# Performance work log

Measured on AMD Instinct MI355X. Metric: run time of the kernel, lower is better.

The kernel has to match this reference:

```python
import jax, jax.numpy as jnp
import numpy as np

ALPHA = 0.2  # LeakyReLU negative slope


def _pair_indices(N):
    # Faithful reproduction of the source's cat(dim=1)+view indexing quirk.
    # a_input[b, i, j, :F]  = h[b, idx(m0)] with m0 = 2*(i*N + j)
    # a_input[b, i, j, F:]  = h[b, idx(m1)] with m1 = m0 + 1
    # idx(m) = m // N            if m <  N*N   (first repeat: h_i blocks)
    #        = (m - N*N) % N     if m >= N*N   (second repeat: h_j tiling)
    i = jnp.arange(N, dtype=jnp.int32)[:, None]
    j = jnp.arange(N, dtype=jnp.int32)[None, :]
    m0 = 2 * (i * N + j)
    m1 = m0 + 1
    NN = N * N
    idx0 = jnp.where(m0 < NN, m0 // N, (m0 - NN) % N)
    idx1 = jnp.where(m1 < NN, m1 // N, (m1 - NN) % N)
    return idx0, idx1  # each [N, N] int32


def reference(inp, W, a):
    # inp: [B, N, Fin], W: [Fin, Fout], a: [2*Fout, 1]
    h = inp @ W                       # [B, N, F]
    B, N, F = h.shape
    a1 = a[:F, 0]                     # [F]
    a2 = a[F:, 0]                     # [F]
    # Decompose additive score: a_input @ a = a1.h_left + a2.h_right
    s1 = h @ a1                       # [B, N]
    s2 = h @ a2                       # [B, N]
    idx0, idx1 = _pair_indices(N)     # [N, N]
    score = s1[:, idx0] + s2[:, idx1]                     # [B, N, N]
    score = jax.nn.leaky_relu(score, negative_slope=ALPHA)
    attn = jax.nn.softmax(score, axis=1)                  # softmax over dim=1 as in source
    # dropout is identity in eval mode (dropout=0.0)
    h_prime = jnp.einsum('bij,bjf->bif', attn, h)         # [B, N, F]
    return jax.nn.elu(h_prime)                            # concat=True -> ELU


def setup_inputs() -> dict:
    B, N, Fin, Fout = 4, 4096, 128, 64
    key = jax.random.key(0)
    k1, k2, k3 = jax.random.split(key, 3)
    inp = jax.random.normal(k1, (B, N, Fin), dtype=jnp.float32)
    # xavier_uniform with gain=1.414
    gain = 1.414
    lim_W = gain * np.sqrt(6.0 / (Fin + Fout))
    W = jax.random.uniform(k2, (Fin, Fout), dtype=jnp.float32, minval=-lim_W, maxval=lim_W)
    lim_a = gain * np.sqrt(6.0 / (2 * Fout + 1))
    a = jax.random.uniform(k3, (2 * Fout, 1), dtype=jnp.float32, minval=-lim_a, maxval=lim_a)
    return {"inp": inp, "W": W, "a": a}
```

## Files before the change

kernel.cpp:

```cpp
#include <hip/hip_runtime.h>
#include <math.h>

#define ALPHA 0.2f

constexpr int BB   = 4;
constexpr int NN_  = 4096;
constexpr int HN   = 2048;
constexpr int FIN  = 128;
constexpr int FF   = 64;
constexpr int ROWS = BB * NN_;

constexpr size_t WS_H  = 0;
constexpr size_t WS_C  = (size_t)ROWS * FF;
constexpr size_t WS_E  = WS_C + ROWS;
constexpr size_t WS_A0 = WS_E + ROWS;
constexpr size_t WS_A1 = WS_A0 + (size_t)BB * FF;
constexpr size_t WS_U  = WS_A1 + (size_t)BB * FF;
constexpr size_t WS_M  = WS_U + (size_t)BB * FF;
constexpr size_t WS_WQ = WS_M + 2 * BB;

__global__ __launch_bounds__(256) void k1_gemm(const float* __restrict__ inp,
                                               const float* __restrict__ W,
                                               const float* __restrict__ a,
                                               float* __restrict__ ws) {
  const int tid  = threadIdx.x;
  const int lane = tid & 63;
  const int wv   = __builtin_amdgcn_readfirstlane(tid >> 6);
  __shared__ float rows_s[32 * FIN];

  float Wreg[FIN];
  #pragma unroll
  for (int k = 0; k < FIN; ++k) Wreg[k] = W[k * FF + lane];
  const float a1 = a[lane];
  const float a2 = a[FF + lane];
  const float asum = a1 + a2;

  const int rowbase = blockIdx.x * 32;
  const float4* src = reinterpret_cast<const float4*>(inp + (size_t)rowbase * FIN);
  float4* dst = reinterpret_cast<float4*>(rows_s);
  #pragma unroll
  for (int i = 0; i < 4; ++i) dst[tid + i * 256] = src[tid + i * 256];
  __syncthreads();

  float* hout = ws + WS_H;
  float* cout = ws + WS_C;
  float* eout = ws + WS_E;

  #pragma unroll
  for (int p = 0; p < 4; ++p) {
    const int lr0 = wv * 8 + 2 * p;
    const float* rp0 = rows_s + lr0 * FIN;
    const float* rp1 = rp0 + FIN;
    float h0 = 0.f, h0b = 0.f, h1 = 0.f, h1b = 0.f;
    #pragma unroll
    for (int k = 0; k < FIN; k += 4) {
      const float4 x0 = *reinterpret_cast<const float4*>(rp0 + k);
      const float4 x1 = *reinterpret_cast<const float4*>(rp1 + k);
      h0  = fmaf(x0.x, Wreg[k],     h0);
      h0b = fmaf(x0.y, Wreg[k + 1], h0b);
      h0  = fmaf(x0.z, Wreg[k + 2], h0);
      h0b = fmaf(x0.w, Wreg[k + 3], h0b);
      h1  = fmaf(x1.x, Wreg[k],     h1);
      h1b = fmaf(x1.y, Wreg[k + 1], h1b);
      h1  = fmaf(x1.z, Wreg[k + 2], h1);
      h1b = fmaf(x1.w, Wreg[k + 3], h1b);
    }
    const float H0 = h0 + h0b;
    const float H1 = h1 + h1b;
    const int r0 = rowbase + lr0;
    hout[(size_t)r0 * FF + lane] = H0;
    hout[(size_t)(r0 + 1) * FF + lane] = H1;

    float c0 = H0 * asum, e0 = H0 * a1;
    float c1 = H1 * asum, e1 = H1 * a2;
    #pragma unroll
    for (int s = 32; s >= 1; s >>= 1) {
      c0 += __shfl_xor(c0, s, 64);
      e0 += __shfl_xor(e0, s, 64);
      c1 += __shfl_xor(c1, s, 64);
      e1 += __shfl_xor(e1, s, 64);
    }
    if (lane == 0) {
      cout[r0] = c0;     eout[r0] = e0;
      cout[r0 + 1] = c1; eout[r0 + 1] = e1;
    }
  }
}

__global__ __launch_bounds__(1024) void k2_stats(float* __restrict__ ws) {
  const int b    = blockIdx.x;
  const int tid  = threadIdx.x;
  const int lane = tid & 63;
  const int w    = tid >> 6;
  const float* c = ws + WS_C + (size_t)b * NN_;
  const float* e = ws + WS_E + (size_t)b * NN_;
  __shared__ float redm[16][2];
  __shared__ float bc[4];

  const float4 cv = reinterpret_cast<const float4*>(c)[tid];
  const float l0 = cv.x > 0.f ? cv.x : ALPHA * cv.x;
  const float l1 = cv.y > 0.f ? cv.y : ALPHA * cv.y;
  const float l2 = cv.z > 0.f ? cv.z : ALPHA * cv.z;
  const float l3 = cv.w > 0.f ? cv.w : ALPHA * cv.w;
  float me = fmaxf(l0, l2), mo = fmaxf(l1, l3);
  #pragma unroll
  for (int s = 32; s >= 1; s >>= 1) {
    me = fmaxf(me, __shfl_xor(me, s, 64));
    mo = fmaxf(mo, __shfl_xor(mo, s, 64));
  }
  if (lane == 0) { redm[w][0] = me; redm[w][1] = mo; }
  __syncthreads();
  if (tid == 0) {
    float M0 = -INFINITY, M1 = -INFINITY;
    for (int i = 0; i < 16; ++i) {
      M0 = fmaxf(M0, redm[i][0]);
      M1 = fmaxf(M1, redm[i][1]);
    }
    bc[0] = M0; bc[1] = M1;
  }
  __syncthreads();
  const float M0 = bc[0], M1 = bc[1];
  float se = __expf(l0 - M0) + __expf(l2 - M0);
  float so = __expf(l1 - M1) + __expf(l3 - M1);
  #pragma unroll
  for (int s = 32; s >= 1; s >>= 1) {
    se += __shfl_xor(se, s, 64);
    so += __shfl_xor(so, s, 64);
  }
  __syncthreads();
  if (lane == 0) { redm[w][0] = se; redm[w][1] = so; }
  __syncthreads();
  if (tid == 0) {
    float P0 = 0.f, P1 = 0.f;
    for (int i = 0; i < 16; ++i) { P0 += redm[i][0]; P1 += redm[i][1]; }
    bc[2] = P0; bc[3] = P1;
    ws[WS_M + 2 * b]     = M0;
    ws[WS_M + 2 * b + 1] = M1;
  }
  __syncthreads();
  const float P0 = bc[2], P1 = bc[3];

  float4* wq = reinterpret_cast<float4*>(ws + WS_WQ) + (size_t)b * HN;
  #pragma unroll
  for (int i = 0; i < 2; ++i) {
    const int jp = tid + i * 1024;
    const float2 ev = reinterpret_cast<const float2*>(e)[jp];
    const float d = ev.x + ev.y;
    const float v = d > 0.f ? d : ALPHA * d;
    const float m0 = fmaxf(M0, v), m1 = fmaxf(M1, v);
    const float eM0 = __expf(M0 - m0), ev0 = __expf(v - m0);
    const float eM1 = __expf(M1 - m1), ev1 = __expf(v - m1);
    const float Z0 = eM0 * P0 + (float)HN * ev0;
    const float Z1 = eM1 * P1 + (float)HN * ev1;
    wq[jp] = make_float4(eM0 / Z0, ev0 / Z0, eM1 / Z1, ev1 / Z1);
  }
  if (tid < FF) {
    ws[WS_A0 + (size_t)b * FF + tid] = 0.f;
    ws[WS_A1 + (size_t)b * FF + tid] = 0.f;
    ws[WS_U  + (size_t)b * FF + tid] = 0.f;
  }
}

constexpr int NSEG = 32;
constexpr int SEGR = 128;

__global__ __launch_bounds__(256) void k3_colsum(float* __restrict__ ws) {
  const int b    = blockIdx.x >> 5;
  const int seg  = blockIdx.x & 31;
  const int tid  = threadIdx.x;
  const int lane = tid & 63;
  const int wv   = __builtin_amdgcn_readfirstlane(tid >> 6);
  const float* h = ws + WS_H + (size_t)b * NN_ * FF;
  const float4* wq = reinterpret_cast<const float4*>(ws + WS_WQ) + (size_t)b * HN;
  __shared__ float accbuf[4][2][64];

  const int j0 = seg * SEGR + wv * 32;
  float accA = 0.f, accU = 0.f;
  #pragma unroll 8
  for (int r = 0; r < 32; ++r) {
    const int j = j0 + r;
    const float hv = h[(size_t)j * FF + lane];
    const float4 q = wq[j & (HN - 1)];
    const float qa = (j < HN) ? q.x : q.z;
    const float qu = (j < HN) ? q.y : q.w;
    accA = fmaf(qa, hv, accA);
    accU = fmaf(qu, hv, accU);
  }
  accbuf[wv][0][lane] = accA;
  accbuf[wv][1][lane] = accU;
  __syncthreads();
  if (tid < 64) {
    const float sA = accbuf[0][0][tid] + accbuf[1][0][tid] + accbuf[2][0][tid] + accbuf[3][0][tid];
    const float sU = accbuf[0][1][tid] + accbuf[1][1][tid] + accbuf[2][1][tid] + accbuf[3][1][tid];
    float* A = ws + ((seg < NSEG / 2) ? WS_A0 : WS_A1) + (size_t)b * FF;
    atomicAdd(&A[tid], sA);
    atomicAdd(ws + WS_U + (size_t)b * FF + tid, sU);
  }
}

__global__ __launch_bounds__(256) void k4_out(const float* __restrict__ ws,
                                              float* __restrict__ out) {
  const int idx = blockIdx.x * 256 + threadIdx.x;
  const int b   = idx >> 16;
  const int rem = idx & 65535;
  const int i   = rem >> 4;
  const int fg  = rem & 15;
  float4 v;
  if (i < HN) {
    const float* c = ws + WS_C + (size_t)b * NN_;
    const float M0 = ws[WS_M + 2 * b];
    const float M1 = ws[WS_M + 2 * b + 1];
    float c0 = c[2 * i], c1 = c[2 * i + 1];
    c0 = c0 > 0.f ? c0 : ALPHA * c0;
    c1 = c1 > 0.f ? c1 : ALPHA * c1;
    const float al = __expf(c0 - M0);
    const float be = __expf(c1 - M1);
    const float4 A0v = reinterpret_cast<const float4*>(ws + WS_A0 + (size_t)b * FF)[fg];
    const float4 A1v = reinterpret_cast<const float4*>(ws + WS_A1 + (size_t)b * FF)[fg];
    v.x = al * A0v.x + be * A1v.x;
    v.y = al * A0v.y + be * A1v.y;
    v.z = al * A0v.z + be * A1v.z;
    v.w = al * A0v.w + be * A1v.w;
  } else {
    v = reinterpret_cast<const float4*>(ws + WS_U + (size_t)b * FF)[fg];
  }
  v.x = v.x > 0.f ? v.x : expm1f(v.x);
  v.y = v.y > 0.f ? v.y : expm1f(v.y);
  v.z = v.z > 0.f ? v.z : expm1f(v.z);
  v.w = v.w > 0.f ? v.w : expm1f(v.w);
  reinterpret_cast<float4*>(out)[idx] = v;
}

extern "C" void kernel_launch(void* const* d_in, const int* in_sizes, int n_in,
                              void* d_out, int out_size, void* d_ws, size_t ws_size,
                              hipStream_t stream) {
  (void)in_sizes; (void)n_in; (void)out_size; (void)ws_size;
  const float* inp = (const float*)d_in[0];
  const float* W   = (const float*)d_in[1];
  const float* a   = (const float*)d_in[2];
  float* out = (float*)d_out;
  float* ws  = (float*)d_ws;

  hipLaunchKernelGGL(k1_gemm,   dim3(ROWS / 32),        dim3(256),  0, stream, inp, W, a, ws);
  hipLaunchKernelGGL(k2_stats,  dim3(BB),               dim3(1024), 0, stream, ws);
  hipLaunchKernelGGL(k3_colsum, dim3(BB * NSEG),        dim3(256),  0, stream, ws);
  hipLaunchKernelGGL(k4_out,    dim3(ROWS * FF / 1024), dim3(256),  0, stream, ws, out);
}
```

Measured before the change: 34.99 us.

## Fuse four kernels into one persistent kernel with global atomic barriers

```diff
diff --git a/kernel.cpp b/kernel.cpp
--- a/kernel.cpp
+++ b/kernel.cpp
@@ -9,141 +9,152 @@
 constexpr int FIN  = 128;
 constexpr int FF   = 64;
 constexpr int ROWS = BB * NN_;
-
-constexpr size_t WS_H  = 0;
-constexpr size_t WS_C  = (size_t)ROWS * FF;
-constexpr size_t WS_E  = WS_C + ROWS;
-constexpr size_t WS_A0 = WS_E + ROWS;
-constexpr size_t WS_A1 = WS_A0 + (size_t)BB * FF;
-constexpr size_t WS_U  = WS_A1 + (size_t)BB * FF;
-constexpr size_t WS_M  = WS_U + (size_t)BB * FF;
-constexpr size_t WS_WQ = WS_M + 2 * BB;
-
-__global__ __launch_bounds__(256) void k1_gemm(const float* __restrict__ inp,
-                                               const float* __restrict__ W,
-                                               const float* __restrict__ a,
-                                               float* __restrict__ ws) {
+constexpr int NBLK = 256;
+
+constexpr size_t WS_H    = 0;
+constexpr size_t WS_C    = (size_t)ROWS * FF;
+constexpr size_t WS_E    = WS_C + ROWS;
+constexpr size_t WS_A0   = WS_E + ROWS;
+constexpr size_t WS_A1   = WS_A0 + (size_t)BB * FF;
+constexpr size_t WS_U    = WS_A1 + (size_t)BB * FF;
+constexpr size_t WS_M    = WS_U + (size_t)BB * FF;
+constexpr size_t WS_WQ   = WS_M + 2 * BB;
+constexpr size_t WS_SYNC = WS_WQ + (size_t)BB * HN * 4;
+
+__device__ __forceinline__ void gbar(int* cnt, int tid) {
+  __syncthreads();
+  if (tid == 0) {
+    __threadfence();
+    atomicAdd(cnt, 1);
+    while (atomicAdd(cnt, 0) < NBLK) __builtin_amdgcn_s_sleep(2);
+    __threadfence();
+  }
+  __syncthreads();
+}
+
+__global__ __launch_bounds__(256) void fused(const float* __restrict__ inp,
+                                             const float* __restrict__ W,
+                                             const float* __restrict__ a,
+                                             float* __restrict__ ws,
+                                             float* __restrict__ out) {
   const int tid  = threadIdx.x;
   const int lane = tid & 63;
   const int wv   = __builtin_amdgcn_readfirstlane(tid >> 6);
-  __shared__ float rows_s[32 * FIN];
-
-  float Wreg[FIN];
-  #pragma unroll
-  for (int k = 0; k < FIN; ++k) Wreg[k] = W[k * FF + lane];
-  const float a1 = a[lane];
-  const float a2 = a[FF + lane];
-  const float asum = a1 + a2;
-
-  const int rowbase = blockIdx.x * 32;
-  const float4* src = reinterpret_cast<const float4*>(inp + (size_t)rowbase * FIN);
-  float4* dst = reinterpret_cast<float4*>(rows_s);
-  #pragma unroll
-  for (int i = 0; i < 4; ++i) dst[tid + i * 256] = src[tid + i * 256];
-  __syncthreads();
-
-  float* hout = ws + WS_H;
-  float* cout = ws + WS_C;
-  float* eout = ws + WS_E;
-
-  #pragma unroll
-  for (int p = 0; p < 4; ++p) {
-    const int lr0 = wv * 8 + 2 * p;
-    const float* rp0 = rows_s + lr0 * FIN;
-    const float* rp1 = rp0 + FIN;
-    float h0 = 0.f, h0b = 0.f, h1 = 0.f, h1b = 0.f;
-    #pragma unroll
-    for (int k = 0; k < FIN; k += 4) {
-      const float4 x0 = *reinterpret_cast<const float4*>(rp0 + k);
-      const float4 x1 = *reinterpret_cast<const float4*>(rp1 + k);
-      h0  = fmaf(x0.x, Wreg[k],     h0);
-      h0b = fmaf(x0.y, Wreg[k + 1], h0b);
-      h0  = fmaf(x0.z, Wreg[k + 2], h0);
-      h0b = fmaf(x0.w, Wreg[k + 3], h0b);
-      h1  = fmaf(x1.x, Wreg[k],     h1);
-      h1b = fmaf(x1.y, Wreg[k + 1], h1b);
-      h1  = fmaf(x1.z, Wreg[k + 2], h1);
-      h1b = fmaf(x1.w, Wreg[k + 3], h1b);
-    }
-    const float H0 = h0 + h0b;
-    const float H1 = h1 + h1b;
-    const int r0 = rowbase + lr0;
-    hout[(size_t)r0 * FF + lane] = H0;
-    hout[(size_t)(r0 + 1) * FF + lane] = H1;
-
-    float c0 = H0 * asum, e0 = H0 * a1;
-    float c1 = H1 * asum, e1 = H1 * a2;
+  const int blk  = blockIdx.x;
+  int* cnt = (int*)(ws + WS_SYNC);
+
+  __shared__ float rows_s[64 * FIN];
+  __shared__ float redm[4][2];
+  __shared__ float accbuf[4][2][64];
+
+  {
+    float Wreg[FIN];
+    #pragma unroll
+    for (int k = 0; k < FIN; ++k) Wreg[k] = W[k * FF + lane];
+    const float a1 = a[lane];
+    const float a2 = a[FF + lane];
+    const float asum = a1 + a2;
+
+    const int rowbase = blk * 64;
+    const float4* src = reinterpret_cast<const float4*>(inp + (size_t)rowbase * FIN);
+    float4* dst = reinterpret_cast<float4*>(rows_s);
+    #pragma unroll
+    for (int i = 0; i < 8; ++i) dst[tid + i * 256] = src[tid + i * 256];
+    __syncthreads();
+
+    if (blk < 3) ws[WS_A0 + (size_t)blk * 256 + tid] = 0.f;
+
+    float* hout = ws + WS_H;
+    float* cout = ws + WS_C;
+    float* eout = ws + WS_E;
+
+    for (int p = 0; p < 8; ++p) {
+      const int lr0 = wv * 16 + 2 * p;
+      const float* rp0 = rows_s + lr0 * FIN;
+      const float* rp1 = rp0 + FIN;
+      float h0 = 0.f, h0b = 0.f, h1 = 0.f, h1b = 0.f;
+      #pragma unroll
+      for (int k = 0; k < FIN; k += 4) {
+        const float4 x0 = *reinterpret_cast<const float4*>(rp0 + k);
+        const float4 x1 = *reinterpret_cast<const float4*>(rp1 + k);
+        h0  = fmaf(x0.x, Wreg[k],     h0);
+        h0b = fmaf(x0.y, Wreg[k + 1], h0b);
+        h0  = fmaf(x0.z, Wreg[k + 2], h0);
+        h0b = fmaf(x0.w, Wreg[k + 3], h0b);
+        h1  = fmaf(x1.x, Wreg[k],     h1);
+        h1b = fmaf(x1.y, Wreg[k + 1], h1b);
+        h1  = fmaf(x1.z, Wreg[k + 2], h1);
+        h1b = fmaf(x1.w, Wreg[k + 3], h1b);
+      }
+      const float H0 = h0 + h0b;
+      const float H1 = h1 + h1b;
+      const int r0 = rowbase + lr0;
+      hout[(size_t)r0 * FF + lane] = H0;
+      hout[(size_t)(r0 + 1) * FF + lane] = H1;
+
+      float c0 = H0 * asum, e0 = H0 * a1;
+      float c1 = H1 * asum, e1 = H1 * a2;
+      #pragma unroll
+      for (int s = 32; s >= 1; s >>= 1) {
+        c0 += __shfl_xor(c0, s, 64);
+        e0 += __shfl_xor(e0, s, 64);
+        c1 += __shfl_xor(c1, s, 64);
+        e1 += __shfl_xor(e1, s, 64);
+      }
+      if (lane == 0) {
+        cout[r0] = c0;     eout[r0] = e0;
+        cout[r0 + 1] = c1; eout[r0 + 1] = e1;
+      }
+    }
+  }
+  gbar(cnt + 0, tid);
+
+  if (blk < 32) {
+    const int b = blk >> 3, slice = blk & 7;
+    const float* c = ws + WS_C + (size_t)b * NN_;
+    const float* e = ws + WS_E + (size_t)b * NN_;
+
+    float lv[16];
+    float me = -INFINITY, mo = -INFINITY;
+    #pragma unroll
+    for (int i = 0; i < 4; ++i) {
+      const float4 cv = reinterpret_cast<const float4*>(c)[tid + i * 256];
+      const float l0 = cv.x > 0.f ? cv.x : ALPHA * cv.x;
+      const float l1 = cv.y > 0.f ? cv.y : ALPHA * cv.y;
+      const float l2 = cv.z > 0.f ? cv.z : ALPHA * cv.z;
+      const float l3 = cv.w > 0.f ? cv.w : ALPHA * cv.w;
+      lv[4*i] = l0; lv[4*i+1] = l1; lv[4*i+2] = l2; lv[4*i+3] = l3;
+      me = fmaxf(me, fmaxf(l0, l2));
+      mo = fmaxf(mo, fmaxf(l1, l3));
+    }
     #pragma unroll
     for (int s = 32; s >= 1; s >>= 1) {
-      c0 += __shfl_xor(c0, s, 64);
-      e0 += __shfl_xor(e0, s, 64);
-      c1 += __shfl_xor(c1, s, 64);
-      e1 += __shfl_xor(e1, s, 64);
-    }
-    if (lane == 0) {
-      cout[r0] = c0;     eout[r0] = e0;
-      cout[r0 + 1] = c1; eout[r0 + 1] = e1;
-    }
-  }
-}
-
-__global__ __launch_bounds__(1024) void k2_stats(float* __restrict__ ws) {
-  const int b    = blockIdx.x;
-  const int tid  = threadIdx.x;
-  const int lane = tid & 63;
-  const int w    = tid >> 6;
-  const float* c = ws + WS_C + (size_t)b * NN_;
-  const float* e = ws + WS_E + (size_t)b * NN_;
-  __shared__ float redm[16][2];
-  __shared__ float bc[4];
-
-  const float4 cv = reinterpret_cast<const float4*>(c)[tid];
-  const float l0 = cv.x > 0.f ? cv.x : ALPHA * cv.x;
-  const float l1 = cv.y > 0.f ? cv.y : ALPHA * cv.y;
-  const float l2 = cv.z > 0.f ? cv.z : ALPHA * cv.z;
-  const float l3 = cv.w > 0.f ? cv.w : ALPHA * cv.w;
-  float me = fmaxf(l0, l2), mo = fmaxf(l1, l3);
-  #pragma unroll
-  for (int s = 32; s >= 1; s >>= 1) {
-    me = fmaxf(me, __shfl_xor(me, s, 64));
-    mo = fmaxf(mo, __shfl_xor(mo, s, 64));
-  }
-  if (lane == 0) { redm[w][0] = me; redm[w][1] = mo; }
-  __syncthreads();
-  if (tid == 0) {
-    float M0 = -INFINITY, M1 = -INFINITY;
-    for (int i = 0; i < 16; ++i) {
-      M0 = fmaxf(M0, redm[i][0]);
-      M1 = fmaxf(M1, redm[i][1]);
-    }
-    bc[0] = M0; bc[1] = M1;
-  }
-  __syncthreads();
-  const float M0 = bc[0], M1 = bc[1];
-  float se = __expf(l0 - M0) + __expf(l2 - M0);
-  float so = __expf(l1 - M1) + __expf(l3 - M1);
-  #pragma unroll
-  for (int s = 32; s >= 1; s >>= 1) {
-    se += __shfl_xor(se, s, 64);
-    so += __shfl_xor(so, s, 64);
-  }
-  __syncthreads();
-  if (lane == 0) { redm[w][0] = se; redm[w][1] = so; }
-  __syncthreads();
-  if (tid == 0) {
-    float P0 = 0.f, P1 = 0.f;
-    for (int i = 0; i < 16; ++i) { P0 += redm[i][0]; P1 += redm[i][1]; }
-    bc[2] = P0; bc[3] = P1;
-    ws[WS_M + 2 * b]     = M0;
-    ws[WS_M + 2 * b + 1] = M1;
-  }
-  __syncthreads();
-  const float P0 = bc[2], P1 = bc[3];
-
-  float4* wq = reinterpret_cast<float4*>(ws + WS_WQ) + (size_t)b * HN;
-  #pragma unroll
-  for (int i = 0; i < 2; ++i) {
-    const int jp = tid + i * 1024;
+      me = fmaxf(me, __shfl_xor(me, s, 64));
+      mo = fmaxf(mo, __shfl_xor(mo, s, 64));
+    }
+    if (lane == 0) { redm[wv][0] = me; redm[wv][1] = mo; }
+    __syncthreads();
+    const float M0 = fmaxf(fmaxf(redm[0][0], redm[1][0]), fmaxf(redm[2][0], redm[3][0]));
+    const float M1 = fmaxf(fmaxf(redm[0][1], redm[1][1]), fmaxf(redm[2][1], redm[3][1]));
+    __syncthreads();
+
+    float se = 0.f, so = 0.f;
+    #pragma unroll
+    for (int i = 0; i < 4; ++i) {
+      se += __expf(lv[4*i]     - M0) + __expf(lv[4*i+2] - M0);
+      so += __expf(lv[4*i + 1] - M1) + __expf(lv[4*i+3] - M1);
+    }
+    #pragma unroll
+    for (int s = 32; s >= 1; s >>= 1) {
+      se += __shfl_xor(se, s, 64);
+      so += __shfl_xor(so, s, 64);
+    }
+    if (lane == 0) { redm[wv][0] = se; redm[wv][1] = so; }
+    __syncthreads();
+    const float P0 = redm[0][0] + redm[1][0] + redm[2][0] + redm[3][0];
+    const float P1 = redm[0][1] + redm[1][1] + redm[2][1] + redm[3][1];
+
+    const int jp = slice * 256 + tid;
     const float2 ev = reinterpret_cast<const float2*>(e)[jp];
     const float d = ev.x + ev.y;
     const float v = d > 0.f ? d : ALPHA * d;
@@ -152,83 +163,76 @@
     const float eM1 = __expf(M1 - m1), ev1 = __expf(v - m1);
     const float Z0 = eM0 * P0 + (float)HN * ev0;
     const float Z1 = eM1 * P1 + (float)HN * ev1;
-    wq[jp] = make_float4(eM0 / Z0, ev0 / Z0, eM1 / Z1, ev1 / Z1);
-  }
-  if (tid < FF) {
-    ws[WS_A0 + (size_t)b * FF + tid] = 0.f;
-    ws[WS_A1 + (size_t)b * FF + tid] = 0.f;
-    ws[WS_U  + (size_t)b * FF + tid] = 0.f;
-  }
-}
-
-constexpr int NSEG = 32;
-constexpr int SEGR = 128;
-
-__global__ __launch_bounds__(256) void k3_colsum(float* __restrict__ ws) {
-  const int b    = blockIdx.x >> 5;
-  const int seg  = blockIdx.x & 31;
-  const int tid  = threadIdx.x;
-  const int lane = tid & 63;
-  const int wv   = __builtin_amdgcn_readfirstlane(tid >> 6);
-  const float* h = ws + WS_H + (size_t)b * NN_ * FF;
-  const float4* wq = reinterpret_cast<const float4*>(ws + WS_WQ) + (size_t)b * HN;
-  __shared__ float accbuf[4][2][64];
-
-  const int j0 = seg * SEGR + wv * 32;
-  float accA = 0.f, accU = 0.f;
-  #pragma unroll 8
-  for (int r = 0; r < 32; ++r) {
-    const int j = j0 + r;
-    const float hv = h[(size_t)j * FF + lane];
-    const float4 q = wq[j & (HN - 1)];
-    const float qa = (j < HN) ? q.x : q.z;
-    const float qu = (j < HN) ? q.y : q.w;
-    accA = fmaf(qa, hv, accA);
-    accU = fmaf(qu, hv, accU);
-  }
-  accbuf[wv][0][lane] = accA;
-  accbuf[wv][1][lane] = accU;
-  __syncthreads();
-  if (tid < 64) {
-    const float sA = accbuf[0][0][tid] + accbuf[1][0][tid] + accbuf[2][0][tid] + accbuf[3][0][tid];
-    const float sU = accbuf[0][1][tid] + accbuf[1][1][tid] + accbuf[2][1][tid] + accbuf[3][1][tid];
-    float* A = ws + ((seg < NSEG / 2) ? WS_A0 : WS_A1) + (size_t)b * FF;
-    atomicAdd(&A[tid], sA);
-    atomicAdd(ws + WS_U + (size_t)b * FF + tid, sU);
-  }
-}
-
-__global__ __launch_bounds__(256) void k4_out(const float* __restrict__ ws,
-                                              float* __restrict__ out) {
-  const int idx = blockIdx.x * 256 + threadIdx.x;
-  const int b   = idx >> 16;
-  const int rem = idx & 65535;
-  const int i   = rem >> 4;
-  const int fg  = rem & 15;
-  float4 v;
-  if (i < HN) {
-    const float* c = ws + WS_C + (size_t)b * NN_;
-    const float M0 = ws[WS_M + 2 * b];
-    const float M1 = ws[WS_M + 2 * b + 1];
-    float c0 = c[2 * i], c1 = c[2 * i + 1];
-    c0 = c0 > 0.f ? c0 : ALPHA * c0;
-    c1 = c1 > 0.f ? c1 : ALPHA * c1;
-    const float al = __expf(c0 - M0);
-    const float be = __expf(c1 - M1);
-    const float4 A0v = reinterpret_cast<const float4*>(ws + WS_A0 + (size_t)b * FF)[fg];
-    const float4 A1v = reinterpret_cast<const float4*>(ws + WS_A1 + (size_t)b * FF)[fg];
-    v.x = al * A0v.x + be * A1v.x;
-    v.y = al * A0v.y + be * A1v.y;
-    v.z = al * A0v.z + be * A1v.z;
-    v.w = al * A0v.w + be * A1v.w;
-  } else {
-    v = reinterpret_cast<const float4*>(ws + WS_U + (size_t)b * FF)[fg];
-  }
-  v.x = v.x > 0.f ? v.x : expm1f(v.x);
-  v.y = v.y > 0.f ? v.y : expm1f(v.y);
-  v.z = v.z > 0.f ? v.z : expm1f(v.z);
-  v.w = v.w > 0.f ? v.w : expm1f(v.w);
-  reinterpret_cast<float4*>(out)[idx] = v;
+    reinterpret_cast<float4*>(ws + WS_WQ)[(size_t)b * HN + jp] =
+        make_float4(eM0 / Z0, ev0 / Z0, eM1 / Z1, ev1 / Z1);
+
+    if (slice == 0 && tid == 0) { ws[WS_M + 2*b] = M0; ws[WS_M + 2*b + 1] = M1; }
+  }
+  gbar(cnt + 1, tid);
+
+  {
+    const int b   = blk >> 6;
+    const int seg = blk & 63;
+    const float* h = ws + WS_H + (size_t)b * NN_ * FF;
+    const float4* wq = reinterpret_cast<const float4*>(ws + WS_WQ) + (size_t)b * HN;
+
+    const int j0 = seg * 64 + wv * 16;
+    float accA = 0.f, accU = 0.f;
+    #pragma unroll 8
+    for (int r = 0; r < 16; ++r) {
+      const int j = j0 + r;
+      const float hv = h[(size_t)j * FF + lane];
+      const float4 q = wq[j & (HN - 1)];
+      const float qa = (seg < 32) ? q.x : q.z;
+      const float qu = (seg < 32) ? q.y : q.w;
+      accA = fmaf(qa, hv, accA);
+      accU = fmaf(qu, hv, accU);
+    }
+    accbuf[wv][0][lane] = accA;
+    accbuf[wv][1][lane] = accU;
+    __syncthreads();
+    if (tid < 64) {
+      const float sA = accbuf[0][0][tid] + accbuf[1][0][tid] + accbuf[2][0][tid] + accbuf[3][0][tid];
+      const float sU = accbuf[0][1][tid] + accbuf[1][1][tid] + accbuf[2][1][tid] + accbuf[3][1][tid];
+      float* A = ws + ((seg < 32) ? WS_A0 : WS_A1) + (size_t)b * FF;
+      atomicAdd(&A[tid], sA);
+      atomicAdd(ws + WS_U + (size_t)b * FF + tid, sU);
+    }
+  }
+  gbar(cnt + 2, tid);
+
+  #pragma unroll
+  for (int it = 0; it < 4; ++it) {
+    const int idx = blk * 1024 + it * 256 + tid;
+    const int b   = idx >> 16;
+    const int rem = idx & 65535;
+    const int i   = rem >> 4;
+    const int fg  = rem & 15;
+    float4 v;
+    if (i < HN) {
+      const float* c = ws + WS_C + (size_t)b * NN_;
+      const float M0 = ws[WS_M + 2 * b];
+      const float M1 = ws[WS_M + 2 * b + 1];
+      float c0 = c[2 * i], c1 = c[2 * i + 1];
+      c0 = c0 > 0.f ? c0 : ALPHA * c0;
+      c1 = c1 > 0.f ? c1 : ALPHA * c1;
+      const float al = __expf(c0 - M0);
+      const float be = __expf(c1 - M1);
+      const float4 A0v = reinterpret_cast<const float4*>(ws + WS_A0 + (size_t)b * FF)[fg];
+      const float4 A1v = reinterpret_cast<const float4*>(ws + WS_A1 + (size_t)b * FF)[fg];
+      v.x = al * A0v.x + be * A1v.x;
+      v.y = al * A0v.y + be * A1v.y;
+      v.z = al * A0v.z + be * A1v.z;
+      v.w = al * A0v.w + be * A1v.w;
+    } else {
+      v = reinterpret_cast<const float4*>(ws + WS_U + (size_t)b * FF)[fg];
+    }
+    v.x = v.x > 0.f ? v.x : expm1f(v.x);
+    v.y = v.y > 0.f ? v.y : expm1f(v.y);
+    v.z = v.z > 0.f ? v.z : expm1f(v.z);
+    v.w = v.w > 0.f ? v.w : expm1f(v.w);
+    reinterpret_cast<float4*>(out)[idx] = v;
+  }
 }
 
 extern "C" void kernel_launch(void* const* d_in, const int* in_sizes, int n_in,
@@ -241,8 +245,6 @@
   float* out = (float*)d_out;
   float* ws  = (float*)d_ws;
 
-  hipLaunchKernelGGL(k1_gemm,   dim3(ROWS / 32),        dim3(256),  0, stream, inp, W, a, ws);
-  hipLaunchKernelGGL(k2_stats,  dim3(BB),               dim3(1024), 0, stream, ws);
-  hipLaunchKernelGGL(k3_colsum, dim3(BB * NSEG),        dim3(256),  0, stream, ws);
-  hipLaunchKernelGGL(k4_out,    dim3(ROWS * FF / 1024), dim3(256),  0, stream, ws, out);
+  hipMemsetAsync((char*)d_ws + WS_SYNC * sizeof(float), 0, 64, stream);
+  hipLaunchKernelGGL(fused, dim3(NBLK), dim3(256), 0, stream, inp, W, a, ws, out);
 }
```

New measurement: 80.87 us. +131.1%, slower.
